# Kernel optimization log

Hardware: AMD Instinct MI355X
Metric: run time of the kernel (lower is better)

## Reference

```python
import jax, jax.numpy as jnp
import numpy as np

N_PROT, N_SUB = 50000, 2000
D_PROT, D_SUB, D_PROJ, KERNEL, N_INT = 256, 256, 128, 16, 64


def setup_inputs() -> dict:
    key = jax.random.key(0)
    ks = jax.random.split(key, 8)
    init = lambda k, shape: jax.random.normal(k, shape, dtype=jnp.float32) * 0.02
    return {
        "prot_node": jax.random.normal(ks[0], (N_PROT, D_PROT), dtype=jnp.float32),
        "sub_node": jax.random.normal(ks[1], (N_SUB, D_SUB), dtype=jnp.float32),
        "int_index": jax.random.randint(ks[2], (N_INT,), 0, N_SUB),
        "Wp": init(ks[3], (D_PROT, D_PROJ)),  # prot_proj weight (in,out layout)
        "bp": jnp.zeros((D_PROJ,), jnp.float32),
        "Ws": init(ks[4], (D_SUB, D_PROJ)),   # sub_proj weight
        "bs": jnp.zeros((D_PROJ,), jnp.float32),
        "wa": init(ks[5], (2 * D_PROJ,)),     # attention_proj weight (out dim 1)
        "ba": jnp.zeros((), jnp.float32),
        "sub_out": init(ks[6], (D_PROJ, D_SUB)),
        "prot_out": init(ks[7], (D_PROJ, D_PROT)),
    }


def reference(prot_node, sub_node, int_index, Wp, bp, Ws, bs, wa, ba, sub_out, prot_out):
    K = KERNEL
    prot_proj = prot_node @ Wp + bp                              # [N, D]
    # reaction potion: sum of projected interacting substrate nodes -> [D]
    reaction = jnp.sum(sub_node[int_index] @ Ws + bs, axis=0)
    num_windows = prot_node.shape[0] - K + 1                     # W
    # attention_proj(concat(window_row, reaction)) splits linearly:
    #   logit = window_row . wa[:D] + reaction . wa[D:] + ba
    # The reaction part is a per-row constant -> compute per-node logits once.
    w1, w2 = wa[:D_PROJ], wa[D_PROJ:]
    g = prot_proj @ w1 + (reaction @ w2 + ba)                    # [N]
    # sliding-window gather indices [W, K]
    idx = jnp.arange(num_windows)[:, None] + jnp.arange(K)[None, :]
    attn = jax.nn.softmax(g[idx], axis=1)                        # [W, K] softmax over window
    local = jnp.einsum('wk,wkd->wd', attn, prot_proj[idx])       # [W, D]
    scores = local + reaction                                    # [W, D]
    # rank windows and pick the best
    top = jnp.argmax(jnp.sum(scores, axis=1))
    top_score = scores[top]                                      # [D]
    # scatter updates back into the node features
    # (set matches torch's non-accumulating fancy-index += for duplicate indices;
    #  the added delta is identical for every row anyway)
    sub_new = sub_node.at[int_index].set(sub_node[int_index] + top_score @ sub_out)
    prot_delta = top_score @ prot_out                            # [D_PROT]
    win = jax.lax.dynamic_slice(prot_node, (top, 0), (K, D_PROT))
    prot_new = jax.lax.dynamic_update_slice(prot_node, win + prot_delta, (top, 0))
    return prot_new, sub_new, int_index
```

## Files before the change

### kernel.cpp

```cpp
#include <hip/hip_runtime.h>
#include <math.h>

#define N_PROT 50000
#define N_SUB  2000
#define D_PROT 256
#define D_SUB  256
#define D_PROJ 128
#define KW     16
#define N_INT  64
#define NWIN   (N_PROT - KW + 1)

#define OUT_SUB (N_PROT * D_PROT)
#define OUT_IDX (OUT_SUB + N_SUB * D_SUB)

#define WS_PACK  0
#define WS_REACT 2
#define WS_CNT   130
#define WS_U1    132
#define WS_U2    388
#define WS_G     644
#define WS_P     (WS_G + N_PROT)

#define PB 1563
#define SB 64
#define NBLK (PB + SB)
#define WBLK ((NWIN + 1023) / 1024)

__global__ __launch_bounds__(256) void k_prep(
    const float* __restrict__ sub_node, const int* __restrict__ int_index,
    const float* __restrict__ Ws, const float* __restrict__ bs,
    const float* __restrict__ Wp, const float* __restrict__ wa,
    float* __restrict__ ws) {
  const int tid = threadIdx.x;
  if (blockIdx.x == 0) {
    __shared__ int   sidx[N_INT];
    __shared__ float ssum[D_SUB];
    if (tid < N_INT) sidx[tid] = int_index[tid];
    __syncthreads();
    float acc = 0.f;
    #pragma unroll 8
    for (int i = 0; i < N_INT; ++i) acc += sub_node[sidx[i] * D_SUB + tid];
    ssum[tid] = acc;
    __syncthreads();
    if (tid < D_PROJ) {
      float r = 64.0f * bs[tid];
      #pragma unroll 8
      for (int d = 0; d < D_SUB; ++d) r = fmaf(ssum[d], Ws[d * D_PROJ + tid], r);
      ws[WS_REACT + tid] = r;
    }
    if (tid == 0) {
      *((unsigned long long*)ws) = 0ull;
      ((unsigned int*)ws)[WS_CNT] = 0u;
    }
  } else {
    __shared__ float swa[D_PROJ];
    if (tid < D_PROJ) swa[tid] = wa[tid];
    __syncthreads();
    float s1 = 0.f, s2 = 0.f;
    const float4* wrow = (const float4*)&Wp[tid * D_PROJ];
    #pragma unroll 8
    for (int j4 = 0; j4 < D_PROJ / 4; ++j4) {
      float4 w = wrow[j4];
      float4 a = *(const float4*)&swa[j4 * 4];
      s1 = fmaf(w.x, a.x, fmaf(w.y, a.y, fmaf(w.z, a.z, fmaf(w.w, a.w, s1))));
      s2 += w.x + w.y + w.z + w.w;
    }
    ws[WS_U1 + tid] = s1;
    ws[WS_U2 + tid] = s2;
  }
}

__global__ __launch_bounds__(256) void k_main(
    const float* __restrict__ prot, const float* __restrict__ sub_node,
    const int* __restrict__ int_index, float* __restrict__ out,
    float* __restrict__ ws) {
  const int tid = threadIdx.x, lane = tid & 63, wave = tid >> 6;
  const int b = blockIdx.x;
  if (b < PB) {
    const float4 c1 = *(const float4*)&ws[WS_U1 + lane * 4];
    const float4 c2 = *(const float4*)&ws[WS_U2 + lane * 4];
    const int rbase = b * 32 + wave * 8;
    if (rbase + 8 <= N_PROT) {
      float4 av[8];
      #pragma unroll
      for (int i = 0; i < 8; ++i)
        av[i] = *(const float4*)&prot[(rbase + i) * D_PROT + lane * 4];
      #pragma unroll
      for (int i = 0; i < 8; ++i)
        *(float4*)&out[(rbase + i) * D_PROT + lane * 4] = av[i];
      #pragma unroll
      for (int i = 0; i < 8; ++i) {
        float g = av[i].x * c1.x + av[i].y * c1.y + av[i].z * c1.z + av[i].w * c1.w;
        float p = av[i].x * c2.x + av[i].y * c2.y + av[i].z * c2.z + av[i].w * c2.w;
        #pragma unroll
        for (int off = 32; off > 0; off >>= 1) {
          g += __shfl_xor(g, off, 64);
          p += __shfl_xor(p, off, 64);
        }
        if (lane == 0) {
          const int r = rbase + i;
          ws[WS_G + r] = g; ws[WS_P + r] = p;
        }
      }
    } else {
      for (int i = 0; i < 8; ++i) {
        const int r = rbase + i;
        if (r >= N_PROT) break;
        const float4 av = *(const float4*)&prot[r * D_PROT + lane * 4];
        *(float4*)&out[r * D_PROT + lane * 4] = av;
        float g = av.x * c1.x + av.y * c1.y + av.z * c1.z + av.w * c1.w;
        float p = av.x * c2.x + av.y * c2.y + av.z * c2.z + av.w * c2.w;
        for (int off = 32; off > 0; off >>= 1) {
          g += __shfl_xor(g, off, 64);
          p += __shfl_xor(p, off, 64);
        }
        if (lane == 0) { ws[WS_G + r] = g; ws[WS_P + r] = p; }
      }
    }
  } else {
    const int sb = b - PB;
    #pragma unroll
    for (int i = 0; i < 8; ++i) {
      const int gi = sb * 2048 + i * 256 + tid;
      if (gi < (N_SUB * D_SUB) / 4)
        *(float4*)&out[OUT_SUB + gi * 4] = *(const float4*)&sub_node[gi * 4];
    }
    if (sb == 0 && tid < N_INT) out[OUT_IDX + tid] = (float)int_index[tid];
  }
}

__global__ __launch_bounds__(1024) void k_finish(
    const float* __restrict__ prot, const float* __restrict__ sub_node,
    const int* __restrict__ int_index, const float* __restrict__ Wp,
    const float* __restrict__ bp, const float* __restrict__ sub_out,
    const float* __restrict__ prot_out, float* __restrict__ ws,
    float* __restrict__ out) {
  __shared__ float sg[1024 + KW], sp[1024 + KW];
  __shared__ unsigned long long wred[16];
  __shared__ int slast;
  const int tid = threadIdx.x;
  const int w0 = blockIdx.x * 1024;
  for (int i = tid; i < 1024 + KW - 1; i += 1024) {
    int idx = w0 + i;
    bool ok = idx < N_PROT;
    sg[i] = ok ? ws[WS_G + idx] : -1e30f;
    sp[i] = ok ? ws[WS_P + idx] : 0.f;
  }
  __syncthreads();
  {
    int w = w0 + tid;
    unsigned long long best = 0ull;
    if (w < NWIN) {
      float m = sg[tid];
      #pragma unroll
      for (int k = 1; k < KW; ++k) m = fmaxf(m, sg[tid + k]);
      float s = 0.f, t = 0.f;
      #pragma unroll
      for (int k = 0; k < KW; ++k) {
        float e = expf(sg[tid + k] - m);
        s += e;
        t = fmaf(e, sp[tid + k], t);
      }
      t /= s;
      unsigned int bb = __float_as_uint(t);
      unsigned int u = bb ^ ((bb & 0x80000000u) ? 0xFFFFFFFFu : 0x80000000u);
      best = ((unsigned long long)u << 32) |
             (unsigned long long)(0xFFFFFFFFu - (unsigned)w);
    }
    #pragma unroll
    for (int off = 32; off > 0; off >>= 1) {
      unsigned long long o = __shfl_xor(best, off, 64);
      if (o > best) best = o;
    }
    if ((tid & 63) == 0) wred[tid >> 6] = best;
  }
  __syncthreads();
  if (tid == 0) {
    unsigned long long b2 = wred[0];
    for (int i = 1; i < 16; ++i) if (wred[i] > b2) b2 = wred[i];
    atomicMax((unsigned long long*)ws, b2);
    __threadfence();
    unsigned int ticket = atomicAdd(&((unsigned int*)ws)[WS_CNT], 1u);
    slast = (ticket == WBLK - 1) ? 1 : 0;
  }
  __syncthreads();
  if (!slast) return;

  __shared__ float aprot[KW][D_PROT];
  __shared__ float attn[KW];
  __shared__ float v[D_PROT];
  __shared__ float part[8][D_PROJ];
  __shared__ float ts[D_PROJ];
  __shared__ float partP[4][D_PROT], partS[4][D_PROT];
  __shared__ float pdelta[D_PROT], sdelta[D_SUB];
  __shared__ int   sidx[N_INT];
  __shared__ int   swtop;
  if (tid == 0) {
    unsigned long long pk = atomicMax((unsigned long long*)ws, 0ull);
    swtop = (int)(0xFFFFFFFFu - (unsigned)(pk & 0xFFFFFFFFull));
  }
  __syncthreads();
  const int wtop = swtop;
  {
    const int row = tid >> 6, c4 = (tid & 63) * 4;
    *(float4*)&aprot[row][c4] = *(const float4*)&prot[(wtop + row) * D_PROT + c4];
  }
  if (tid < N_INT) sidx[tid] = int_index[tid];
  if (tid == 0) {
    float m = ws[WS_G + wtop];
    for (int k = 1; k < KW; ++k) m = fmaxf(m, ws[WS_G + wtop + k]);
    float e[KW], s = 0.f;
    for (int k = 0; k < KW; ++k) { e[k] = expf(ws[WS_G + wtop + k] - m); s += e[k]; }
    for (int k = 0; k < KW; ++k) attn[k] = e[k] / s;
  }
  __syncthreads();
  if (tid < D_PROT) {
    float a = 0.f;
    #pragma unroll
    for (int k = 0; k < KW; ++k) a = fmaf(attn[k], aprot[k][tid], a);
    v[tid] = a;
  }
  __syncthreads();
  {
    const int j = tid & 127, s = tid >> 7;
    float p = 0.f;
    const float* wp = Wp + (s * 32) * D_PROJ + j;
    #pragma unroll 8
    for (int d = 0; d < 32; ++d) p = fmaf(v[s * 32 + d], wp[d * D_PROJ], p);
    part[s][j] = p;
  }
  __syncthreads();
  if (tid < D_PROJ) {
    float a = ws[WS_REACT + tid] + bp[tid];
    #pragma unroll
    for (int s = 0; s < 8; ++s) a += part[s][tid];
    ts[tid] = a;
  }
  __syncthreads();
  {
    const int d = tid & 255, s = tid >> 8;
    float pp = 0.f, ss = 0.f;
    #pragma unroll 8
    for (int j = 0; j < 32; ++j) {
      const float t = ts[s * 32 + j];
      pp = fmaf(t, prot_out[(s * 32 + j) * D_PROT + d], pp);
      ss = fmaf(t, sub_out[(s * 32 + j) * D_SUB + d], ss);
    }
    partP[s][d] = pp; partS[s][d] = ss;
  }
  __syncthreads();
  if (tid < D_PROT) {
    pdelta[tid] = partP[0][tid] + partP[1][tid] + partP[2][tid] + partP[3][tid];
    sdelta[tid] = partS[0][tid] + partS[1][tid] + partS[2][tid] + partS[3][tid];
  }
  __syncthreads();
  {
    const int row = tid >> 6, c4 = (tid & 63) * 4;
    float4 a = *(float4*)&aprot[row][c4];
    float4 d = *(float4*)&pdelta[c4];
    a.x += d.x; a.y += d.y; a.z += d.z; a.w += d.w;
    *(float4*)&out[(wtop + row) * D_PROT + c4] = a;
  }
  #pragma unroll
  for (int it = 0; it < 4; ++it) {
    const int f = tid + it * 1024;
    const int row = f >> 6, c4 = (f & 63) * 4;
    const int rr = sidx[row];
    float4 sv = *(const float4*)&sub_node[rr * D_SUB + c4];
    float4 d = *(float4*)&sdelta[c4];
    sv.x += d.x; sv.y += d.y; sv.z += d.z; sv.w += d.w;
    *(float4*)&out[OUT_SUB + rr * D_SUB + c4] = sv;
  }
}

extern "C" void kernel_launch(void* const* d_in, const int* in_sizes, int n_in,
                              void* d_out, int out_size, void* d_ws, size_t ws_size,
                              hipStream_t stream) {
  const float* prot     = (const float*)d_in[0];
  const float* sub      = (const float*)d_in[1];
  const int*   idx      = (const int*)d_in[2];
  const float* Wp       = (const float*)d_in[3];
  const float* bp       = (const float*)d_in[4];
  const float* Ws       = (const float*)d_in[5];
  const float* bs       = (const float*)d_in[6];
  const float* wa       = (const float*)d_in[7];
  const float* sub_out  = (const float*)d_in[9];
  const float* prot_out = (const float*)d_in[10];
  float* out = (float*)d_out;
  float* ws  = (float*)d_ws;

  k_prep<<<2, 256, 0, stream>>>(sub, idx, Ws, bs, Wp, wa, ws);
  k_main<<<NBLK, 256, 0, stream>>>(prot, sub, idx, out, ws);
  k_finish<<<WBLK, 1024, 0, stream>>>(prot, sub, idx, Wp, bp, sub_out, prot_out,
                                      ws, out);
}
```

Before: 151.9 us.

## Fuse window scoring and patch into main kernel via per-chunk completion counters

Merges the streaming copy, window softmax/argmax and final patch into one kernel. Per-chunk atomic counters let the last block finishing a 1024-window chunk score it, and the last chunk finisher applies the patch, so the separate finish launch and its tail go away. Also skips copying substrate rows that the patch overwrites (via a bitmask built in the init kernel), uses nontemporal stores for the substrate copy, and prefetches the output weights in the reaction block. In exchange the code depends on fine-grained atomics and fences for correctness, and the serialized chunk and patch work now sits at the end of the big kernel.

```diff
diff --git a/kernel.cpp b/kernel.cpp
--- a/kernel.cpp
+++ b/kernel.cpp
@@ -15,79 +15,283 @@
 
 #define WS_PACK  0
 #define WS_REACT 2
-#define WS_CNT   130
-#define WS_U1    132
-#define WS_U2    388
-#define WS_G     644
+#define WS_CNT2  130
+#define WS_CCNT  132
+#define WS_MASK  184
+#define WS_U1    248
+#define WS_U2    504
+#define WS_G     760
 #define WS_P     (WS_G + N_PROT)
 
-#define PB 1563
-#define SB 64
-#define NBLK (PB + SB)
-#define WBLK ((NWIN + 1023) / 1024)
-
-__global__ __launch_bounds__(256) void k_prep(
-    const float* __restrict__ sub_node, const int* __restrict__ int_index,
-    const float* __restrict__ Ws, const float* __restrict__ bs,
+#define PB   1563
+#define SB   64
+#define NBLK (1 + SB + PB)
+#define NWCH 49
+#define EXPC(c) ((c) == NWCH - 1 ? 27 : 33)
+
+typedef float v4f __attribute__((ext_vector_type(4)));
+
+union SMem {
+  struct { int sidx[N_INT]; float ssum[D_SUB]; } react;
+  struct { float sg[1024 + KW]; float sp[1024 + KW]; unsigned long long wred[4]; } win;
+  struct {
+    float aprot[KW][D_PROT];
+    float attn[KW];
+    float v[D_PROT];
+    float part[2][D_PROJ];
+    float ts[D_PROJ];
+    float pdelta[D_PROT];
+    float sdelta[D_SUB];
+    int   sidx[N_INT];
+  } patch;
+};
+
+__global__ __launch_bounds__(256) void k_init(
     const float* __restrict__ Wp, const float* __restrict__ wa,
+    const int* __restrict__ int_index, float* __restrict__ ws) {
+  const int tid = threadIdx.x;
+  __shared__ unsigned smask[63];
+  __shared__ float swa[D_PROJ];
+  if (tid < 63) smask[tid] = 0u;
+  if (tid < D_PROJ) swa[tid] = wa[tid];
+  __syncthreads();
+  if (tid < N_INT) {
+    const int ii = int_index[tid];
+    atomicOr(&smask[ii >> 5], 1u << (ii & 31));
+  }
+  __syncthreads();
+  if (tid < 63) ((unsigned*)ws)[WS_MASK + tid] = smask[tid];
+  if (tid == 0) {
+    *((unsigned long long*)ws) = 0ull;
+    ((unsigned*)ws)[WS_CNT2] = 0u;
+  }
+  if (tid < NWCH) ((unsigned*)ws)[WS_CCNT + tid] = 0u;
+  float s1 = 0.f, s2 = 0.f;
+  const v4f* wrow = (const v4f*)&Wp[tid * D_PROJ];
+  #pragma unroll 8
+  for (int j4 = 0; j4 < D_PROJ / 4; ++j4) {
+    v4f w = wrow[j4];
+    v4f a = *(const v4f*)&swa[j4 * 4];
+    s1 = fmaf(w.x, a.x, fmaf(w.y, a.y, fmaf(w.z, a.z, fmaf(w.w, a.w, s1))));
+    s2 += w.x + w.y + w.z + w.w;
+  }
+  ws[WS_U1 + tid] = s1;
+  ws[WS_U2 + tid] = s2;
+}
+
+__device__ void do_chunk(SMem& sm, const int tid, const int lane,
+                         const int wave, const int chunk,
+                         float* __restrict__ ws) {
+  const int w0 = chunk * 1024;
+  for (int i = tid; i < 1024 + KW - 1; i += 256) {
+    const int idx = w0 + i;
+    const bool ok = idx < N_PROT;
+    sm.win.sg[i] = ok ? ws[WS_G + idx] : -1e30f;
+    sm.win.sp[i] = ok ? ws[WS_P + idx] : 0.f;
+  }
+  __syncthreads();
+  unsigned long long best = 0ull;
+  #pragma unroll
+  for (int it = 0; it < 4; ++it) {
+    const int i = tid + it * 256;
+    const int w = w0 + i;
+    if (w < NWIN) {
+      float m = sm.win.sg[i];
+      #pragma unroll
+      for (int k = 1; k < KW; ++k) m = fmaxf(m, sm.win.sg[i + k]);
+      float s = 0.f, t = 0.f;
+      #pragma unroll
+      for (int k = 0; k < KW; ++k) {
+        float e = expf(sm.win.sg[i + k] - m);
+        s += e;
+        t = fmaf(e, sm.win.sp[i + k], t);
+      }
+      t /= s;
+      unsigned int bb = __float_as_uint(t);
+      unsigned int u = bb ^ ((bb & 0x80000000u) ? 0xFFFFFFFFu : 0x80000000u);
+      unsigned long long cand = ((unsigned long long)u << 32) |
+                                (unsigned long long)(0xFFFFFFFFu - (unsigned)w);
+      if (cand > best) best = cand;
+    }
+  }
+  #pragma unroll
+  for (int off = 32; off > 0; off >>= 1) {
+    unsigned long long o = __shfl_xor(best, off, 64);
+    if (o > best) best = o;
+  }
+  if (lane == 0) sm.win.wred[wave] = best;
+  __syncthreads();
+  if (tid == 0) {
+    unsigned long long b2 = sm.win.wred[0];
+    for (int i = 1; i < 4; ++i) if (sm.win.wred[i] > b2) b2 = sm.win.wred[i];
+    atomicMax((unsigned long long*)ws, b2);
+  }
+  __syncthreads();
+}
+
+__device__ void do_patch(
+    SMem& sm, const int tid,
+    const float* __restrict__ prot, const float* __restrict__ sub_node,
+    const int* __restrict__ int_index, const float* __restrict__ Wp,
+    const float* __restrict__ bp, const float* __restrict__ sub_out,
+    const float* __restrict__ prot_out, float* __restrict__ ws,
+    float* __restrict__ out) {
+  __shared__ int s_wtop;
+  if (tid == 0) {
+    unsigned long long pk = atomicMax((unsigned long long*)ws, 0ull);
+    s_wtop = (int)(0xFFFFFFFFu - (unsigned)(pk & 0xFFFFFFFFull));
+  }
+  __syncthreads();
+  const int wtop = s_wtop;
+  #pragma unroll
+  for (int it = 0; it < 4; ++it) {
+    const int f = tid + it * 256;
+    const int row = f >> 6, c4 = (f & 63) * 4;
+    *(v4f*)&sm.patch.aprot[row][c4] =
+        *(const v4f*)&prot[(wtop + row) * D_PROT + c4];
+  }
+  if (tid < N_INT) sm.patch.sidx[tid] = int_index[tid];
+  if (tid == 0) {
+    float m = ws[WS_G + wtop];
+    for (int k = 1; k < KW; ++k) m = fmaxf(m, ws[WS_G + wtop + k]);
+    float e[KW], s = 0.f;
+    for (int k = 0; k < KW; ++k) { e[k] = expf(ws[WS_G + wtop + k] - m); s += e[k]; }
+    for (int k = 0; k < KW; ++k) sm.patch.attn[k] = e[k] / s;
+  }
+  __syncthreads();
+  {
+    float a = 0.f;
+    #pragma unroll
+    for (int k = 0; k < KW; ++k) a = fmaf(sm.patch.attn[k], sm.patch.aprot[k][tid], a);
+    sm.patch.v[tid] = a;
+  }
+  __syncthreads();
+  {
+    const int j = tid & 127, sl = tid >> 7;
+    float p = 0.f;
+    const float* wp = Wp + (sl * 128) * D_PROJ + j;
+    #pragma unroll 8
+    for (int d = 0; d < 128; ++d) p = fmaf(sm.patch.v[sl * 128 + d], wp[d * D_PROJ], p);
+    sm.patch.part[sl][j] = p;
+  }
+  __syncthreads();
+  if (tid < D_PROJ)
+    sm.patch.ts[tid] = ws[WS_REACT + tid] + bp[tid] +
+                       sm.patch.part[0][tid] + sm.patch.part[1][tid];
+  __syncthreads();
+  {
+    float pp = 0.f, ss = 0.f;
+    #pragma unroll 8
+    for (int j = 0; j < D_PROJ; ++j) {
+      const float t = sm.patch.ts[j];
+      pp = fmaf(t, prot_out[j * D_PROT + tid], pp);
+      ss = fmaf(t, sub_out[j * D_SUB + tid], ss);
+    }
+    sm.patch.pdelta[tid] = pp; sm.patch.sdelta[tid] = ss;
+  }
+  __syncthreads();
+  #pragma unroll
+  for (int it = 0; it < 4; ++it) {
+    const int f = tid + it * 256;
+    const int row = f >> 6, c4 = (f & 63) * 4;
+    v4f a = *(v4f*)&sm.patch.aprot[row][c4];
+    v4f d = *(v4f*)&sm.patch.pdelta[c4];
+    a.x += d.x; a.y += d.y; a.z += d.z; a.w += d.w;
+    *(v4f*)&out[(wtop + row) * D_PROT + c4] = a;
+  }
+  #pragma unroll
+  for (int it = 0; it < 16; ++it) {
+    const int f = tid + it * 256;
+    const int row = f >> 6, c4 = (f & 63) * 4;
+    const int rr = sm.patch.sidx[row];
+    v4f sv = *(const v4f*)&sub_node[rr * D_SUB + c4];
+    v4f d = *(v4f*)&sm.patch.sdelta[c4];
+    sv.x += d.x; sv.y += d.y; sv.z += d.z; sv.w += d.w;
+    *(v4f*)&out[OUT_SUB + rr * D_SUB + c4] = sv;
+  }
+}
+
+__global__ __launch_bounds__(256) void k_fused(
+    const float* __restrict__ prot, const float* __restrict__ sub_node,
+    const int* __restrict__ int_index, const float* __restrict__ Wp,
+    const float* __restrict__ bp, const float* __restrict__ Ws,
+    const float* __restrict__ bs, const float* __restrict__ sub_out,
+    const float* __restrict__ prot_out, float* __restrict__ out,
     float* __restrict__ ws) {
-  const int tid = threadIdx.x;
-  if (blockIdx.x == 0) {
-    __shared__ int   sidx[N_INT];
-    __shared__ float ssum[D_SUB];
-    if (tid < N_INT) sidx[tid] = int_index[tid];
+  __shared__ SMem sm;
+  __shared__ int s_t2, s_nown, s_own[2];
+  const int tid = threadIdx.x, lane = tid & 63, wave = tid >> 6;
+  const int b = blockIdx.x;
+
+  if (b >= 1 && b <= SB) {
+    const int sb = b - 1;
+    const unsigned* mask = (const unsigned*)ws + WS_MASK;
+    #pragma unroll
+    for (int i = 0; i < 8; ++i) {
+      const int gi = sb * 2048 + i * 256 + tid;
+      if (gi < (N_SUB * D_SUB) / 4) {
+        const int row = gi >> 6;
+        if (!((mask[row >> 5] >> (row & 31)) & 1u))
+          __builtin_nontemporal_store(*(const v4f*)&sub_node[gi * 4],
+                                      (v4f*)&out[OUT_SUB + gi * 4]);
+      }
+    }
+    return;
+  }
+
+  if (b == 0) {
+    if (tid < N_INT) {
+      const int ii = int_index[tid];
+      sm.react.sidx[tid] = ii;
+      out[OUT_IDX + tid] = (float)ii;
+    }
     __syncthreads();
     float acc = 0.f;
     #pragma unroll 8
-    for (int i = 0; i < N_INT; ++i) acc += sub_node[sidx[i] * D_SUB + tid];
-    ssum[tid] = acc;
+    for (int i = 0; i < N_INT; ++i) acc += sub_node[sm.react.sidx[i] * D_SUB + tid];
+    sm.react.ssum[tid] = acc;
     __syncthreads();
     if (tid < D_PROJ) {
       float r = 64.0f * bs[tid];
       #pragma unroll 8
-      for (int d = 0; d < D_SUB; ++d) r = fmaf(ssum[d], Ws[d * D_PROJ + tid], r);
+      for (int d = 0; d < D_SUB; ++d) r = fmaf(sm.react.ssum[d], Ws[d * D_PROJ + tid], r);
       ws[WS_REACT + tid] = r;
     }
+    float wsum = 0.f;
+    for (int i = tid; i < (D_PROJ * D_PROT) / 4; i += 256) {
+      v4f a = ((const v4f*)prot_out)[i];
+      v4f c = ((const v4f*)sub_out)[i];
+      wsum += a.x + c.x;
+    }
+    asm volatile("" :: "v"(wsum));
+    __syncthreads();
     if (tid == 0) {
-      *((unsigned long long*)ws) = 0ull;
-      ((unsigned int*)ws)[WS_CNT] = 0u;
-    }
-  } else {
-    __shared__ float swa[D_PROJ];
-    if (tid < D_PROJ) swa[tid] = wa[tid];
+      unsigned old = __hip_atomic_fetch_add(&((unsigned*)ws)[WS_CNT2], 1u,
+                                            __ATOMIC_RELEASE,
+                                            __HIP_MEMORY_SCOPE_AGENT);
+      s_t2 = (int)old + 1;
+    }
     __syncthreads();
-    float s1 = 0.f, s2 = 0.f;
-    const float4* wrow = (const float4*)&Wp[tid * D_PROJ];
-    #pragma unroll 8
-    for (int j4 = 0; j4 < D_PROJ / 4; ++j4) {
-      float4 w = wrow[j4];
-      float4 a = *(const float4*)&swa[j4 * 4];
-      s1 = fmaf(w.x, a.x, fmaf(w.y, a.y, fmaf(w.z, a.z, fmaf(w.w, a.w, s1))));
-      s2 += w.x + w.y + w.z + w.w;
-    }
-    ws[WS_U1 + tid] = s1;
-    ws[WS_U2 + tid] = s2;
-  }
-}
-
-__global__ __launch_bounds__(256) void k_main(
-    const float* __restrict__ prot, const float* __restrict__ sub_node,
-    const int* __restrict__ int_index, float* __restrict__ out,
-    float* __restrict__ ws) {
-  const int tid = threadIdx.x, lane = tid & 63, wave = tid >> 6;
-  const int b = blockIdx.x;
-  if (b < PB) {
-    const float4 c1 = *(const float4*)&ws[WS_U1 + lane * 4];
-    const float4 c2 = *(const float4*)&ws[WS_U2 + lane * 4];
-    const int rbase = b * 32 + wave * 8;
+    if (s_t2 != NWCH + 1) return;
+    __builtin_amdgcn_fence(__ATOMIC_ACQUIRE, "agent");
+    do_patch(sm, tid, prot, sub_node, int_index, Wp, bp, sub_out, prot_out,
+             ws, out);
+    return;
+  }
+
+  const int sbid = b - 1 - SB;
+  {
+    const v4f c1 = *(const v4f*)&ws[WS_U1 + lane * 4];
+    const v4f c2 = *(const v4f*)&ws[WS_U2 + lane * 4];
+    const int rbase = sbid * 32 + wave * 8;
     if (rbase + 8 <= N_PROT) {
-      float4 av[8];
+      v4f av[8];
       #pragma unroll
       for (int i = 0; i < 8; ++i)
-        av[i] = *(const float4*)&prot[(rbase + i) * D_PROT + lane * 4];
+        av[i] = *(const v4f*)&prot[(rbase + i) * D_PROT + lane * 4];
       #pragma unroll
       for (int i = 0; i < 8; ++i)
-        *(float4*)&out[(rbase + i) * D_PROT + lane * 4] = av[i];
+        *(v4f*)&out[(rbase + i) * D_PROT + lane * 4] = av[i];
       #pragma unroll
       for (int i = 0; i < 8; ++i) {
         float g = av[i].x * c1.x + av[i].y * c1.y + av[i].z * c1.z + av[i].w * c1.w;
@@ -106,8 +310,8 @@
       for (int i = 0; i < 8; ++i) {
         const int r = rbase + i;
         if (r >= N_PROT) break;
-        const float4 av = *(const float4*)&prot[r * D_PROT + lane * 4];
-        *(float4*)&out[r * D_PROT + lane * 4] = av;
+        const v4f av = *(const v4f*)&prot[r * D_PROT + lane * 4];
+        *(v4f*)&out[r * D_PROT + lane * 4] = av;
         float g = av.x * c1.x + av.y * c1.y + av.z * c1.z + av.w * c1.w;
         float p = av.x * c2.x + av.y * c2.y + av.z * c2.z + av.w * c2.w;
         for (int off = 32; off > 0; off >>= 1) {
@@ -117,160 +321,41 @@
         if (lane == 0) { ws[WS_G + r] = g; ws[WS_P + r] = p; }
       }
     }
-  } else {
-    const int sb = b - PB;
-    #pragma unroll
-    for (int i = 0; i < 8; ++i) {
-      const int gi = sb * 2048 + i * 256 + tid;
-      if (gi < (N_SUB * D_SUB) / 4)
-        *(float4*)&out[OUT_SUB + gi * 4] = *(const float4*)&sub_node[gi * 4];
-    }
-    if (sb == 0 && tid < N_INT) out[OUT_IDX + tid] = (float)int_index[tid];
-  }
-}
-
-__global__ __launch_bounds__(1024) void k_finish(
-    const float* __restrict__ prot, const float* __restrict__ sub_node,
-    const int* __restrict__ int_index, const float* __restrict__ Wp,
-    const float* __restrict__ bp, const float* __restrict__ sub_out,
-    const float* __restrict__ prot_out, float* __restrict__ ws,
-    float* __restrict__ out) {
-  __shared__ float sg[1024 + KW], sp[1024 + KW];
-  __shared__ unsigned long long wred[16];
-  __shared__ int slast;
-  const int tid = threadIdx.x;
-  const int w0 = blockIdx.x * 1024;
-  for (int i = tid; i < 1024 + KW - 1; i += 1024) {
-    int idx = w0 + i;
-    bool ok = idx < N_PROT;
-    sg[i] = ok ? ws[WS_G + idx] : -1e30f;
-    sp[i] = ok ? ws[WS_P + idx] : 0.f;
-  }
-  __syncthreads();
-  {
-    int w = w0 + tid;
-    unsigned long long best = 0ull;
-    if (w < NWIN) {
-      float m = sg[tid];
-      #pragma unroll
-      for (int k = 1; k < KW; ++k) m = fmaxf(m, sg[tid + k]);
-      float s = 0.f, t = 0.f;
-      #pragma unroll
-      for (int k = 0; k < KW; ++k) {
-        float e = expf(sg[tid + k] - m);
-        s += e;
-        t = fmaf(e, sp[tid + k], t);
-      }
-      t /= s;
-      unsigned int bb = __float_as_uint(t);
-      unsigned int u = bb ^ ((bb & 0x80000000u) ? 0xFFFFFFFFu : 0x80000000u);
-      best = ((unsigned long long)u << 32) |
-             (unsigned long long)(0xFFFFFFFFu - (unsigned)w);
-    }
-    #pragma unroll
-    for (int off = 32; off > 0; off >>= 1) {
-      unsigned long long o = __shfl_xor(best, off, 64);
-      if (o > best) best = o;
-    }
-    if ((tid & 63) == 0) wred[tid >> 6] = best;
-  }
-  __syncthreads();
-  if (tid == 0) {
-    unsigned long long b2 = wred[0];
-    for (int i = 1; i < 16; ++i) if (wred[i] > b2) b2 = wred[i];
-    atomicMax((unsigned long long*)ws, b2);
-    __threadfence();
-    unsigned int ticket = atomicAdd(&((unsigned int*)ws)[WS_CNT], 1u);
-    slast = (ticket == WBLK - 1) ? 1 : 0;
-  }
-  __syncthreads();
-  if (!slast) return;
-
-  __shared__ float aprot[KW][D_PROT];
-  __shared__ float attn[KW];
-  __shared__ float v[D_PROT];
-  __shared__ float part[8][D_PROJ];
-  __shared__ float ts[D_PROJ];
-  __shared__ float partP[4][D_PROT], partS[4][D_PROT];
-  __shared__ float pdelta[D_PROT], sdelta[D_SUB];
-  __shared__ int   sidx[N_INT];
-  __shared__ int   swtop;
-  if (tid == 0) {
-    unsigned long long pk = atomicMax((unsigned long long*)ws, 0ull);
-    swtop = (int)(0xFFFFFFFFu - (unsigned)(pk & 0xFFFFFFFFull));
-  }
-  __syncthreads();
-  const int wtop = swtop;
-  {
-    const int row = tid >> 6, c4 = (tid & 63) * 4;
-    *(float4*)&aprot[row][c4] = *(const float4*)&prot[(wtop + row) * D_PROT + c4];
-  }
-  if (tid < N_INT) sidx[tid] = int_index[tid];
-  if (tid == 0) {
-    float m = ws[WS_G + wtop];
-    for (int k = 1; k < KW; ++k) m = fmaxf(m, ws[WS_G + wtop + k]);
-    float e[KW], s = 0.f;
-    for (int k = 0; k < KW; ++k) { e[k] = expf(ws[WS_G + wtop + k] - m); s += e[k]; }
-    for (int k = 0; k < KW; ++k) attn[k] = e[k] / s;
-  }
-  __syncthreads();
-  if (tid < D_PROT) {
-    float a = 0.f;
-    #pragma unroll
-    for (int k = 0; k < KW; ++k) a = fmaf(attn[k], aprot[k][tid], a);
-    v[tid] = a;
-  }
-  __syncthreads();
-  {
-    const int j = tid & 127, s = tid >> 7;
-    float p = 0.f;
-    const float* wp = Wp + (s * 32) * D_PROJ + j;
-    #pragma unroll 8
-    for (int d = 0; d < 32; ++d) p = fmaf(v[s * 32 + d], wp[d * D_PROJ], p);
-    part[s][j] = p;
-  }
-  __syncthreads();
-  if (tid < D_PROJ) {
-    float a = ws[WS_REACT + tid] + bp[tid];
-    #pragma unroll
-    for (int s = 0; s < 8; ++s) a += part[s][tid];
-    ts[tid] = a;
-  }
-  __syncthreads();
-  {
-    const int d = tid & 255, s = tid >> 8;
-    float pp = 0.f, ss = 0.f;
-    #pragma unroll 8
-    for (int j = 0; j < 32; ++j) {
-      const float t = ts[s * 32 + j];
-      pp = fmaf(t, prot_out[(s * 32 + j) * D_PROT + d], pp);
-      ss = fmaf(t, sub_out[(s * 32 + j) * D_SUB + d], ss);
-    }
-    partP[s][d] = pp; partS[s][d] = ss;
-  }
-  __syncthreads();
-  if (tid < D_PROT) {
-    pdelta[tid] = partP[0][tid] + partP[1][tid] + partP[2][tid] + partP[3][tid];
-    sdelta[tid] = partS[0][tid] + partS[1][tid] + partS[2][tid] + partS[3][tid];
-  }
-  __syncthreads();
-  {
-    const int row = tid >> 6, c4 = (tid & 63) * 4;
-    float4 a = *(float4*)&aprot[row][c4];
-    float4 d = *(float4*)&pdelta[c4];
-    a.x += d.x; a.y += d.y; a.z += d.z; a.w += d.w;
-    *(float4*)&out[(wtop + row) * D_PROT + c4] = a;
-  }
-  #pragma unroll
-  for (int it = 0; it < 4; ++it) {
-    const int f = tid + it * 1024;
-    const int row = f >> 6, c4 = (f & 63) * 4;
-    const int rr = sidx[row];
-    float4 sv = *(const float4*)&sub_node[rr * D_SUB + c4];
-    float4 d = *(float4*)&sdelta[c4];
-    sv.x += d.x; sv.y += d.y; sv.z += d.z; sv.w += d.w;
-    *(float4*)&out[OUT_SUB + rr * D_SUB + c4] = sv;
-  }
+  }
+
+  __syncthreads();
+  if (tid == 0) {
+    unsigned* ccnt = (unsigned*)ws + WS_CCNT;
+    const int c1 = sbid >> 5;
+    int n = 0, o0 = -1, o1 = -1;
+    unsigned o = __hip_atomic_fetch_add(&ccnt[c1], 1u, __ATOMIC_RELEASE,
+                                        __HIP_MEMORY_SCOPE_AGENT);
+    if ((int)o == EXPC(c1) - 1) { o0 = c1; n = 1; }
+    if ((sbid & 31) == 0 && c1 > 0) {
+      o = __hip_atomic_fetch_add(&ccnt[c1 - 1], 1u, __ATOMIC_RELEASE,
+                                 __HIP_MEMORY_SCOPE_AGENT);
+      if ((int)o == EXPC(c1 - 1) - 1) { if (n) o1 = c1 - 1; else o0 = c1 - 1; ++n; }
+    }
+    s_nown = n; s_own[0] = o0; s_own[1] = o1;
+  }
+  __syncthreads();
+  const int nown = s_nown;
+  if (nown == 0) return;
+  __builtin_amdgcn_fence(__ATOMIC_ACQUIRE, "agent");
+  for (int i = 0; i < nown; ++i)
+    do_chunk(sm, tid, lane, wave, s_own[i], ws);
+
+  if (tid == 0) {
+    unsigned old = __hip_atomic_fetch_add(&((unsigned*)ws)[WS_CNT2], (unsigned)nown,
+                                          __ATOMIC_RELEASE,
+                                          __HIP_MEMORY_SCOPE_AGENT);
+    s_t2 = (int)old + nown;
+  }
+  __syncthreads();
+  if (s_t2 != NWCH + 1) return;
+  __builtin_amdgcn_fence(__ATOMIC_ACQUIRE, "agent");
+  do_patch(sm, tid, prot, sub_node, int_index, Wp, bp, sub_out, prot_out,
+           ws, out);
 }
 
 extern "C" void kernel_launch(void* const* d_in, const int* in_sizes, int n_in,
@@ -289,8 +374,7 @@
   float* out = (float*)d_out;
   float* ws  = (float*)d_ws;
 
-  k_prep<<<2, 256, 0, stream>>>(sub, idx, Ws, bs, Wp, wa, ws);
-  k_main<<<NBLK, 256, 0, stream>>>(prot, sub, idx, out, ws);
-  k_finish<<<WBLK, 1024, 0, stream>>>(prot, sub, idx, Wp, bp, sub_out, prot_out,
-                                      ws, out);
-}
+  k_init<<<1, 256, 0, stream>>>(Wp, wa, idx, ws);
+  k_fused<<<NBLK, 256, 0, stream>>>(prot, sub, idx, Wp, bp, Ws, bs,
+                                    sub_out, prot_out, out, ws);
+}
```

After: 221.9 us. 46.1% more time.

## Fold prep kernel into main and finish kernels to drop a launch

Applied to the files above, without the earlier changes.

The separate k_prep launch goes away. Each k_main protein block now recomputes the Wp·wa and Wp row-sum vectors into shared memory. The reaction vector (the gathered sub_node sum times Ws) is recomputed redundantly by every k_finish block, and workspace counter init moves into a k_main sub block. This removes one kernel launch and its serialization gap. The cost is redundant Wp reads (128 KB per block, mostly L2 hits) across about 1563 blocks and extra prologue work in every finish block.

```diff
diff --git a/kernel.cpp b/kernel.cpp
--- a/kernel.cpp
+++ b/kernel.cpp
@@ -14,11 +14,8 @@
 #define OUT_IDX (OUT_SUB + N_SUB * D_SUB)
 
 #define WS_PACK  0
-#define WS_REACT 2
 #define WS_CNT   130
-#define WS_U1    132
-#define WS_U2    388
-#define WS_G     644
+#define WS_G     136
 #define WS_P     (WS_G + N_PROT)
 
 #define PB 1563
@@ -26,68 +23,44 @@
 #define NBLK (PB + SB)
 #define WBLK ((NWIN + 1023) / 1024)
 
-__global__ __launch_bounds__(256) void k_prep(
-    const float* __restrict__ sub_node, const int* __restrict__ int_index,
-    const float* __restrict__ Ws, const float* __restrict__ bs,
-    const float* __restrict__ Wp, const float* __restrict__ wa,
-    float* __restrict__ ws) {
-  const int tid = threadIdx.x;
-  if (blockIdx.x == 0) {
-    __shared__ int   sidx[N_INT];
-    __shared__ float ssum[D_SUB];
-    if (tid < N_INT) sidx[tid] = int_index[tid];
-    __syncthreads();
-    float acc = 0.f;
-    #pragma unroll 8
-    for (int i = 0; i < N_INT; ++i) acc += sub_node[sidx[i] * D_SUB + tid];
-    ssum[tid] = acc;
-    __syncthreads();
-    if (tid < D_PROJ) {
-      float r = 64.0f * bs[tid];
-      #pragma unroll 8
-      for (int d = 0; d < D_SUB; ++d) r = fmaf(ssum[d], Ws[d * D_PROJ + tid], r);
-      ws[WS_REACT + tid] = r;
-    }
-    if (tid == 0) {
-      *((unsigned long long*)ws) = 0ull;
-      ((unsigned int*)ws)[WS_CNT] = 0u;
-    }
-  } else {
-    __shared__ float swa[D_PROJ];
-    if (tid < D_PROJ) swa[tid] = wa[tid];
-    __syncthreads();
-    float s1 = 0.f, s2 = 0.f;
-    const float4* wrow = (const float4*)&Wp[tid * D_PROJ];
-    #pragma unroll 8
-    for (int j4 = 0; j4 < D_PROJ / 4; ++j4) {
-      float4 w = wrow[j4];
-      float4 a = *(const float4*)&swa[j4 * 4];
-      s1 = fmaf(w.x, a.x, fmaf(w.y, a.y, fmaf(w.z, a.z, fmaf(w.w, a.w, s1))));
-      s2 += w.x + w.y + w.z + w.w;
-    }
-    ws[WS_U1 + tid] = s1;
-    ws[WS_U2 + tid] = s2;
-  }
-}
+typedef float v4f __attribute__((ext_vector_type(4)));
 
 __global__ __launch_bounds__(256) void k_main(
     const float* __restrict__ prot, const float* __restrict__ sub_node,
-    const int* __restrict__ int_index, float* __restrict__ out,
+    const int* __restrict__ int_index, const float* __restrict__ Wp,
+    const float* __restrict__ wa, float* __restrict__ out,
     float* __restrict__ ws) {
   const int tid = threadIdx.x, lane = tid & 63, wave = tid >> 6;
   const int b = blockIdx.x;
   if (b < PB) {
-    const float4 c1 = *(const float4*)&ws[WS_U1 + lane * 4];
-    const float4 c2 = *(const float4*)&ws[WS_U2 + lane * 4];
+    __shared__ float swa[D_PROJ];
+    __shared__ float su1[D_PROT], su2[D_PROT];
+    if (tid < D_PROJ) swa[tid] = wa[tid];
+    __syncthreads();
+    {
+      float s1 = 0.f, s2 = 0.f;
+      const v4f* wrow = (const v4f*)&Wp[tid * D_PROJ];
+      #pragma unroll 8
+      for (int j4 = 0; j4 < D_PROJ / 4; ++j4) {
+        v4f w = wrow[j4];
+        v4f a = *(const v4f*)&swa[j4 * 4];
+        s1 = fmaf(w.x, a.x, fmaf(w.y, a.y, fmaf(w.z, a.z, fmaf(w.w, a.w, s1))));
+        s2 += w.x + w.y + w.z + w.w;
+      }
+      su1[tid] = s1; su2[tid] = s2;
+    }
+    __syncthreads();
+    const v4f c1 = *(const v4f*)&su1[lane * 4];
+    const v4f c2 = *(const v4f*)&su2[lane * 4];
     const int rbase = b * 32 + wave * 8;
     if (rbase + 8 <= N_PROT) {
-      float4 av[8];
+      v4f av[8];
       #pragma unroll
       for (int i = 0; i < 8; ++i)
-        av[i] = *(const float4*)&prot[(rbase + i) * D_PROT + lane * 4];
+        av[i] = *(const v4f*)&prot[(rbase + i) * D_PROT + lane * 4];
       #pragma unroll
       for (int i = 0; i < 8; ++i)
-        *(float4*)&out[(rbase + i) * D_PROT + lane * 4] = av[i];
+        *(v4f*)&out[(rbase + i) * D_PROT + lane * 4] = av[i];
       #pragma unroll
       for (int i = 0; i < 8; ++i) {
         float g = av[i].x * c1.x + av[i].y * c1.y + av[i].z * c1.z + av[i].w * c1.w;
@@ -106,8 +79,8 @@
       for (int i = 0; i < 8; ++i) {
         const int r = rbase + i;
         if (r >= N_PROT) break;
-        const float4 av = *(const float4*)&prot[r * D_PROT + lane * 4];
-        *(float4*)&out[r * D_PROT + lane * 4] = av;
+        const v4f av = *(const v4f*)&prot[r * D_PROT + lane * 4];
+        *(v4f*)&out[r * D_PROT + lane * 4] = av;
         float g = av.x * c1.x + av.y * c1.y + av.z * c1.z + av.w * c1.w;
         float p = av.x * c2.x + av.y * c2.y + av.z * c2.z + av.w * c2.w;
         for (int off = 32; off > 0; off >>= 1) {
@@ -123,22 +96,59 @@
     for (int i = 0; i < 8; ++i) {
       const int gi = sb * 2048 + i * 256 + tid;
       if (gi < (N_SUB * D_SUB) / 4)
-        *(float4*)&out[OUT_SUB + gi * 4] = *(const float4*)&sub_node[gi * 4];
-    }
-    if (sb == 0 && tid < N_INT) out[OUT_IDX + tid] = (float)int_index[tid];
+        *(v4f*)&out[OUT_SUB + gi * 4] = *(const v4f*)&sub_node[gi * 4];
+    }
+    if (sb == 0) {
+      if (tid < N_INT) out[OUT_IDX + tid] = (float)int_index[tid];
+      if (tid == 0) {
+        *((unsigned long long*)ws) = 0ull;
+        ((unsigned int*)ws)[WS_CNT] = 0u;
+      }
+    }
   }
 }
 
 __global__ __launch_bounds__(1024) void k_finish(
     const float* __restrict__ prot, const float* __restrict__ sub_node,
     const int* __restrict__ int_index, const float* __restrict__ Wp,
-    const float* __restrict__ bp, const float* __restrict__ sub_out,
+    const float* __restrict__ bp, const float* __restrict__ Ws,
+    const float* __restrict__ bs, const float* __restrict__ sub_out,
     const float* __restrict__ prot_out, float* __restrict__ ws,
     float* __restrict__ out) {
   __shared__ float sg[1024 + KW], sp[1024 + KW];
   __shared__ unsigned long long wred[16];
   __shared__ int slast;
+  __shared__ int   sidx[N_INT];
+  __shared__ float ssum[D_SUB];
+  __shared__ float rpart[8][D_PROJ];
+  __shared__ float sreact[D_PROJ];
   const int tid = threadIdx.x;
+
+  if (tid < N_INT) sidx[tid] = int_index[tid];
+  __syncthreads();
+  if (tid < D_SUB) {
+    float acc = 0.f;
+    #pragma unroll 8
+    for (int i = 0; i < N_INT; ++i) acc += sub_node[sidx[i] * D_SUB + tid];
+    ssum[tid] = acc;
+  }
+  __syncthreads();
+  {
+    const int j = tid & 127, sl = tid >> 7;
+    float p = 0.f;
+    const float* wsp = Ws + (sl * 32) * D_PROJ + j;
+    #pragma unroll 8
+    for (int d = 0; d < 32; ++d) p = fmaf(ssum[sl * 32 + d], wsp[d * D_PROJ], p);
+    rpart[sl][j] = p;
+  }
+  __syncthreads();
+  if (tid < D_PROJ) {
+    float r = 64.0f * bs[tid];
+    #pragma unroll
+    for (int s = 0; s < 8; ++s) r += rpart[s][tid];
+    sreact[tid] = r;
+  }
+
   const int w0 = blockIdx.x * 1024;
   for (int i = tid; i < 1024 + KW - 1; i += 1024) {
     int idx = w0 + i;
@@ -193,7 +203,6 @@
   __shared__ float ts[D_PROJ];
   __shared__ float partP[4][D_PROT], partS[4][D_PROT];
   __shared__ float pdelta[D_PROT], sdelta[D_SUB];
-  __shared__ int   sidx[N_INT];
   __shared__ int   swtop;
   if (tid == 0) {
     unsigned long long pk = atomicMax((unsigned long long*)ws, 0ull);
@@ -203,9 +212,8 @@
   const int wtop = swtop;
   {
     const int row = tid >> 6, c4 = (tid & 63) * 4;
-    *(float4*)&aprot[row][c4] = *(const float4*)&prot[(wtop + row) * D_PROT + c4];
-  }
-  if (tid < N_INT) sidx[tid] = int_index[tid];
+    *(v4f*)&aprot[row][c4] = *(const v4f*)&prot[(wtop + row) * D_PROT + c4];
+  }
   if (tid == 0) {
     float m = ws[WS_G + wtop];
     for (int k = 1; k < KW; ++k) m = fmaxf(m, ws[WS_G + wtop + k]);
@@ -231,7 +239,7 @@
   }
   __syncthreads();
   if (tid < D_PROJ) {
-    float a = ws[WS_REACT + tid] + bp[tid];
+    float a = sreact[tid] + bp[tid];
     #pragma unroll
     for (int s = 0; s < 8; ++s) a += part[s][tid];
     ts[tid] = a;
@@ -256,20 +264,20 @@
   __syncthreads();
   {
     const int row = tid >> 6, c4 = (tid & 63) * 4;
-    float4 a = *(float4*)&aprot[row][c4];
-    float4 d = *(float4*)&pdelta[c4];
+    v4f a = *(v4f*)&aprot[row][c4];
+    v4f d = *(v4f*)&pdelta[c4];
     a.x += d.x; a.y += d.y; a.z += d.z; a.w += d.w;
-    *(float4*)&out[(wtop + row) * D_PROT + c4] = a;
+    *(v4f*)&out[(wtop + row) * D_PROT + c4] = a;
   }
   #pragma unroll
   for (int it = 0; it < 4; ++it) {
     const int f = tid + it * 1024;
     const int row = f >> 6, c4 = (f & 63) * 4;
     const int rr = sidx[row];
-    float4 sv = *(const float4*)&sub_node[rr * D_SUB + c4];
-    float4 d = *(float4*)&sdelta[c4];
+    v4f sv = *(const v4f*)&sub_node[rr * D_SUB + c4];
+    v4f d = *(v4f*)&sdelta[c4];
     sv.x += d.x; sv.y += d.y; sv.z += d.z; sv.w += d.w;
-    *(float4*)&out[OUT_SUB + rr * D_SUB + c4] = sv;
+    *(v4f*)&out[OUT_SUB + rr * D_SUB + c4] = sv;
   }
 }
 
@@ -289,8 +297,7 @@
   float* out = (float*)d_out;
   float* ws  = (float*)d_ws;
 
-  k_prep<<<2, 256, 0, stream>>>(sub, idx, Ws, bs, Wp, wa, ws);
-  k_main<<<NBLK, 256, 0, stream>>>(prot, sub, idx, out, ws);
-  k_finish<<<WBLK, 1024, 0, stream>>>(prot, sub, idx, Wp, bp, sub_out, prot_out,
-                                      ws, out);
+  k_main<<<NBLK, 256, 0, stream>>>(prot, sub, idx, Wp, wa, out, ws);
+  k_finish<<<WBLK, 1024, 0, stream>>>(prot, sub, idx, Wp, bp, Ws, bs,
+                                      sub_out, prot_out, ws, out);
 }
```

Result: slower. 160.8 us (+5.8%).
